# Performance work log

Measured on AMD Instinct MI355X. Metric: run time of the kernel, lower is better.

The kernel has to match this reference:

```python
import jax, jax.numpy as jnp
import numpy as np

SQRT_QKV_DIM = 8.0  # sqrt(qkv_dim=64)


def setup_inputs() -> dict:
    key = jax.random.key(0)
    ks = jax.random.split(key, 8)
    B, H, T, M, d, hid = 4, 16, 512, 512, 64, 16
    return {
        "q": jax.random.normal(ks[0], (B, H, T, d), dtype=jnp.float32),
        "k": jax.random.normal(ks[1], (B, H, M, d), dtype=jnp.float32),
        "v": jax.random.normal(ks[2], (B, H, M, d), dtype=jnp.float32),
        "D_TM": jax.random.uniform(ks[3], (B, T, M), dtype=jnp.float32),
        "mix1_weight": jax.random.uniform(ks[4], (H, 2, hid), minval=-0.7071, maxval=0.7071, dtype=jnp.float32),
        "mix1_bias": jax.random.uniform(ks[5], (H, hid), minval=-0.7071, maxval=0.7071, dtype=jnp.float32),
        "mix2_weight": jax.random.uniform(ks[6], (H, hid, 1), minval=-0.25, maxval=0.25, dtype=jnp.float32),
        "mix2_bias": jax.random.uniform(ks[7], (H, 1), minval=-0.25, maxval=0.25, dtype=jnp.float32),
    }


def reference(q, k, v, D_TM, mix1_weight, mix1_bias, mix2_weight, mix2_bias):
    B, H, T, d = q.shape
    Mc = k.shape[2]
    # scaled dot-product score: (B,H,T,M)
    dot_score = jnp.einsum("bhtd,bhmd->bhtm", q, k) / SQRT_QKV_DIM
    # per-head 2->hidden->1 MLP mixing dot score and distance bias.
    # Avoid explicit stack: linear layer over the 2 score channels expands as
    # dot*W1[:,0,:] + D*W1[:,1,:].  ms1: (B,H,T,M,hid)
    w1_dot = mix1_weight[:, 0, :][None, :, None, None, :]   # (1,H,1,1,hid)
    w1_dist = mix1_weight[:, 1, :][None, :, None, None, :]
    ms1 = (dot_score[..., None] * w1_dot
           + D_TM[:, None, :, :, None] * w1_dist
           + mix1_bias[None, :, None, None, :])
    ms1 = jax.nn.relu(ms1)
    # hidden -> 1: mixed_scores (B,H,T,M)
    mixed = jnp.einsum("bhtmc,hc->bhtm", ms1, mix2_weight[:, :, 0])
    mixed = mixed + mix2_bias[:, 0][None, :, None, None]
    weights = jax.nn.softmax(mixed, axis=3)
    out = jnp.einsum("bhtm,bhmd->bhtd", weights, v)   # (B,H,T,d)
    return out.transpose(0, 2, 1, 3).reshape(B, T, H * d)
```

## Files before the change

### kernel.cpp

```cpp
#include <hip/hip_runtime.h>
#include <stdint.h>

typedef __attribute__((ext_vector_type(8))) short short8;
typedef __attribute__((ext_vector_type(4))) float floatx4;

#define MFMA(a, b, c) __builtin_amdgcn_mfma_f32_16x16x32_bf16(a, b, c, 0, 0, 0)

union Frag { uint32_t u[4]; short8 s; };

__device__ __forceinline__ void packsplit(float a, float b, uint32_t& hi, uint32_t& lo) {
    uint32_t ua = __float_as_uint(a), ub = __float_as_uint(b);
    uint32_t ha = ua & 0xFFFF0000u, hb = ub & 0xFFFF0000u;
    float ra = a - __uint_as_float(ha);
    float rb = b - __uint_as_float(hb);
    hi = __builtin_amdgcn_perm(ub, ua, 0x07060302u);
    lo = __builtin_amdgcn_perm(__float_as_uint(rb), __float_as_uint(ra), 0x07060302u);
}

__device__ __forceinline__ float fexp2(float x) {
#if __has_builtin(__builtin_amdgcn_exp2f)
    return __builtin_amdgcn_exp2f(x);
#else
    return exp2f(x);
#endif
}

__device__ __forceinline__ void bar_lds() {
    asm volatile("s_waitcnt lgkmcnt(0)" ::: "memory");
    __builtin_amdgcn_s_barrier();
    __builtin_amdgcn_sched_barrier(0);
}


__global__ __launch_bounds__(512)
void msmha_flash(const float* __restrict__ qg, const float* __restrict__ kg,
                 const float* __restrict__ vg, const float* __restrict__ Dg,
                 const float* __restrict__ m1w, const float* __restrict__ m1b,
                 const float* __restrict__ m2w, const float* __restrict__ m2b,
                 float* __restrict__ outg) {
    __shared__ __align__(16) uint32_t sm[18432];
    __shared__ __align__(16) float4 wlds[16];

    const int tid   = threadIdx.x;
    const int w     = tid >> 6;
    const int group = w >> 2;
    const int gw    = w & 3;
    const int lane  = tid & 63;
    const int col   = lane & 15;
    const int quad  = lane >> 4;
    const int gtid  = tid & 255;

    const int bid = blockIdx.x;
    const int wgT = bid >> 6;
    const int bh  = bid & 63;
    const int h   = bh & 15;
    const int b   = bh >> 4;
    const int t0g = wgT * 64;

    const size_t base = (size_t)bh * 512 * 64;
    const float LOG2E = 1.4426950408889634f;

    if (tid < 16) {
        const float w1d = m1w[h * 32 + tid];
        const float w1s = m1w[h * 32 + 16 + tid];
        const float b1  = m1b[h * 16 + tid];
        const float w2  = m2w[h * 16 + tid];
        wlds[tid] = make_float4(w1d * (0.125f * LOG2E), w1s * LOG2E, b1 * LOG2E, 0.5f * w2);
    }

    const int ml0  = gtid >> 4;
    const int k4   = gtid & 15;
    const int dgrp = gtid & 15;
    const int m4   = gtid >> 4;
    const int cpV  = (2 * m4 + 8 * ((dgrp >> 1) & 3)) & 31;
    const int rsel = col >> 3;

    const int gb = group * 9216;
    uint32_t* KH = sm + gb;
    uint32_t* KL = sm + gb + 2304;
    uint32_t* VH = sm + gb + 4608;
    uint32_t* VL = sm + gb + 6912;

    const int moff = group * 256;
    const float* kc = kg + base + (size_t)moff * 64;
    const float* vc = vg + base + (size_t)moff * 64;
    const float* Dc = Dg + ((size_t)b * 512 + t0g + gw * 16 + col) * 512 + moff + quad * 4;

    float4 kp[4];
#pragma unroll
    for (int it = 0; it < 4; ++it)
        kp[it] = *(const float4*)(kc + (size_t)(ml0 + it * 16) * 64 + k4 * 4);

    float sA = 0.f, sB = 0.f, sC = 0.f;
#pragma unroll 1
    for (int c = 0; c < 16; ++c) {
        const float w2 = m2w[h * 16 + c];
        sA = fmaf(w2, m1w[h * 32 + c], sA);
        sB = fmaf(w2, m1w[h * 32 + 16 + c], sB);
        sC = fmaf(w2, m1b[h * 16 + c], sC);
    }
    const float Ac = sA * (0.0625f * LOG2E);
    const float Bc = sB * (0.5f * LOG2E);
    const float Cc = fmaf(0.5f, sC, m2b[h]) * LOG2E;

    Frag qh[2], ql[2];
    {
        const float* qrow = qg + base + (size_t)(t0g + gw * 16 + col) * 64;
#pragma unroll
        for (int ks = 0; ks < 2; ++ks) {
            const float4 f0 = *(const float4*)(qrow + ks * 32 + quad * 8);
            const float4 f1 = *(const float4*)(qrow + ks * 32 + quad * 8 + 4);
            packsplit(f0.x, f0.y, qh[ks].u[0], ql[ks].u[0]);
            packsplit(f0.z, f0.w, qh[ks].u[1], ql[ks].u[1]);
            packsplit(f1.x, f1.y, qh[ks].u[2], ql[ks].u[2]);
            packsplit(f1.z, f1.w, qh[ks].u[3], ql[ks].u[3]);
        }
    }

    float run_m = -3.0e38f, run_l = 0.f;
    floatx4 oacc[4];
#pragma unroll
    for (int dt = 0; dt < 4; ++dt) oacc[dt] = floatx4{0.f, 0.f, 0.f, 0.f};

#pragma unroll
    for (int mc = 0; mc < 4; ++mc) {
        float4 vp[4], dp[4];
#pragma unroll
        for (int i = 0; i < 4; ++i)
            vp[i] = *(const float4*)(vc + (size_t)(mc * 64 + 4 * m4 + i) * 64 + dgrp * 4);
#pragma unroll
        for (int mt = 0; mt < 4; ++mt)
            dp[mt] = *(const float4*)(Dc + mc * 64 + mt * 16);

#pragma unroll
        for (int it = 0; it < 4; ++it) {
            uint32_t h0, l0, h1, l1;
            packsplit(kp[it].x, kp[it].y, h0, l0);
            packsplit(kp[it].z, kp[it].w, h1, l1);
            const int ml = ml0 + it * 16;
            *(uint2*)(KH + ml * 36 + 2 * k4) = make_uint2(h0, h1);
            *(uint2*)(KL + ml * 36 + 2 * k4) = make_uint2(l0, l1);
        }
        if (mc < 3) {
            const float* kn = kc + (size_t)(mc + 1) * 64 * 64;
#pragma unroll
            for (int it = 0; it < 4; ++it)
                kp[it] = *(const float4*)(kn + (size_t)(ml0 + it * 16) * 64 + k4 * 4);
        }
        bar_lds();

        floatx4 sc[4];
        __builtin_amdgcn_s_setprio(1);
#pragma unroll
        for (int mt = 0; mt < 4; ++mt) {
            floatx4 acc = {0.f, 0.f, 0.f, 0.f};
#pragma unroll
            for (int ks = 0; ks < 2; ++ks) {
                const int ro = (mt * 16 + col) * 36 + 16 * ks + 4 * quad;
                Frag ah, al;
                ah.s = *(const short8*)(KH + ro);
                al.s = *(const short8*)(KL + ro);
                acc = MFMA(ah.s, qh[ks].s, acc);
                acc = MFMA(ah.s, ql[ks].s, acc);
                acc = MFMA(al.s, qh[ks].s, acc);
            }
            sc[mt] = acc;
        }
        __builtin_amdgcn_s_setprio(0);

#pragma unroll
        for (int jj = 0; jj < 4; ++jj) {
            uint32_t h0, l0, h1, l1;
            packsplit(((const float*)&vp[0])[jj], ((const float*)&vp[1])[jj], h0, l0);
            packsplit(((const float*)&vp[2])[jj], ((const float*)&vp[3])[jj], h1, l1);
            const int d = 4 * dgrp + jj;
            *(uint2*)(VH + d * 36 + cpV) = make_uint2(h0, h1);
            *(uint2*)(VL + d * 36 + cpV) = make_uint2(l0, l1);
        }

        float dvf[16];
#pragma unroll
        for (int mt = 0; mt < 4; ++mt) {
            dvf[mt * 4 + 0] = dp[mt].x; dvf[mt * 4 + 1] = dp[mt].y;
            dvf[mt * 4 + 2] = dp[mt].z; dvf[mt * 4 + 3] = dp[mt].w;
        }
        float mix[16];
#pragma unroll
        for (int e = 0; e < 16; ++e) mix[e] = fmaf(dvf[e], Bc, Cc);
#pragma unroll 4
        for (int c = 0; c < 16; ++c) {
            const float4 wv = wlds[c];
#pragma unroll
            for (int mt = 0; mt < 4; ++mt)
#pragma unroll
                for (int r = 0; r < 4; ++r) {
                    const float hh = fmaf(sc[mt][r], wv.x, fmaf(dvf[mt * 4 + r], wv.y, wv.z));
                    mix[mt * 4 + r] = fmaf(fabsf(hh), wv.w, mix[mt * 4 + r]);
                }
        }
#pragma unroll
        for (int mt = 0; mt < 4; ++mt)
#pragma unroll
            for (int r = 0; r < 4; ++r)
                sc[mt][r] = fmaf(sc[mt][r], Ac, mix[mt * 4 + r]);

        float cmx = -3.0e38f;
#pragma unroll
        for (int mt = 0; mt < 4; ++mt)
#pragma unroll
            for (int r = 0; r < 4; ++r) cmx = fmaxf(cmx, sc[mt][r]);
        cmx = fmaxf(cmx, __shfl_xor(cmx, 16, 64));
        cmx = fmaxf(cmx, __shfl_xor(cmx, 32, 64));
        const float nm    = fmaxf(run_m, cmx);
        const float scale = fexp2(run_m - nm);
        float csum = 0.f;
#pragma unroll
        for (int mt = 0; mt < 4; ++mt)
#pragma unroll
            for (int r = 0; r < 4; ++r) {
                const float p = fexp2(sc[mt][r] - nm);
                sc[mt][r] = p;
                csum += p;
            }
        csum += __shfl_xor(csum, 16, 64);
        csum += __shfl_xor(csum, 32, 64);
        run_l = fmaf(run_l, scale, csum);
        run_m = nm;
        float sOT[4];
#pragma unroll
        for (int r = 0; r < 4; ++r) sOT[r] = __shfl(scale, quad * 4 + r, 64);
#pragma unroll
        for (int dt = 0; dt < 4; ++dt)
#pragma unroll
            for (int r = 0; r < 4; ++r) oacc[dt][r] *= sOT[r];

        bar_lds();

        const int prow = (gw * 16 + col) * 36;
#pragma unroll
        for (int mt = 0; mt < 4; ++mt) {
            uint32_t h0, l0, h1, l1;
            packsplit(sc[mt][0], sc[mt][1], h0, l0);
            packsplit(sc[mt][2], sc[mt][3], h1, l1);
            *(uint2*)(KH + prow + mt * 8 + 2 * quad) = make_uint2(h0, h1);
            *(uint2*)(KL + prow + mt * 8 + 2 * quad) = make_uint2(l0, l1);
        }

        __builtin_amdgcn_s_setprio(1);
#pragma unroll
        for (int ks = 0; ks < 2; ++ks) {
            const int po = prow + 16 * ks + 4 * quad;
            Frag pah, pal;
            pah.s = *(const short8*)(KH + po);
            pal.s = *(const short8*)(KL + po);
#pragma unroll
            for (int dt = 0; dt < 4; ++dt) {
                const int cbd = ((16 * ks + 4 * quad) + 8 * ((2 * dt + rsel) & 3)) & 31;
                const int vo = (dt * 16 + col) * 36 + cbd;
                Frag bhv, blv;
                bhv.s = *(const short8*)(VH + vo);
                blv.s = *(const short8*)(VL + vo);
                oacc[dt] = MFMA(pah.s, bhv.s, oacc[dt]);
                oacc[dt] = MFMA(pah.s, blv.s, oacc[dt]);
                oacc[dt] = MFMA(pal.s, bhv.s, oacc[dt]);
            }
        }
        __builtin_amdgcn_s_setprio(0);

        bar_lds();
    }

    float* smf = (float*)sm;
    if (group == 1) {
        if (quad == 0) {
            smf[13376 + gw * 16 + col] = run_m;
            smf[13440 + gw * 16 + col] = run_l;
        }
        const int t = gw * 16 + quad * 4;
#pragma unroll
        for (int dt = 0; dt < 4; ++dt)
#pragma unroll
            for (int r = 0; r < 4; ++r)
                smf[9216 + (t + r) * 65 + dt * 16 + col] = oacc[dt][r];
    }
    bar_lds();
    if (group == 0) {
        const float m1c = smf[13376 + gw * 16 + col];
        const float l1c = smf[13440 + gw * 16 + col];
        const float M   = fmaxf(run_m, m1c);
        const float s0  = fexp2(run_m - M);
        const float s1  = fexp2(m1c - M);
        const float rdn = 1.f / fmaf(run_l, s0, l1c * s1);
        float s0T[4], s1T[4], rdT[4];
#pragma unroll
        for (int r = 0; r < 4; ++r) {
            s0T[r] = __shfl(s0, quad * 4 + r, 64);
            s1T[r] = __shfl(s1, quad * 4 + r, 64);
            rdT[r] = __shfl(rdn, quad * 4 + r, 64);
        }
        const int t = gw * 16 + quad * 4;
        const size_t obase = ((size_t)b * 512 + t0g + t) * 1024 + h * 64 + col;
#pragma unroll
        for (int dt = 0; dt < 4; ++dt)
#pragma unroll
            for (int r = 0; r < 4; ++r) {
                const float o1 = smf[9216 + (t + r) * 65 + dt * 16 + col];
                outg[obase + (size_t)r * 1024 + dt * 16] =
                    fmaf(oacc[dt][r], s0T[r], o1 * s1T[r]) * rdT[r];
            }
    }
}

extern "C" void kernel_launch(void* const* d_in, const int* in_sizes, int n_in,
                              void* d_out, int out_size, void* d_ws, size_t ws_size,
                              hipStream_t stream) {
    const float* q   = (const float*)d_in[0];
    const float* k   = (const float*)d_in[1];
    const float* v   = (const float*)d_in[2];
    const float* dtm = (const float*)d_in[3];
    const float* m1w = (const float*)d_in[4];
    const float* m1b = (const float*)d_in[5];
    const float* m2w = (const float*)d_in[6];
    const float* m2b = (const float*)d_in[7];
    float* out = (float*)d_out;

    dim3 grid(4 * 16 * 8);
    dim3 block(512);
    msmha_flash<<<grid, block, 0, stream>>>(q, k, v, dtm, m1w, m1b, m2w, m2b, out);
}
```

Before: 136.9 us.

## Swizzle K/P LDS tiles, pack MLP math into float2, drop loop-end barrier

The K and P tiles in LDS switch from a padded stride-36 layout to an XOR-swizzled stride-32 layout, which shrinks shared memory while still aiming to avoid bank conflicts. K loading is reassigned so each wave writes exactly the K rows it later overwrites with its own P rows. That makes the per-iteration trailing barrier unnecessary, so it moves out of the loop. The per-element score MLP, max and scaling are rewritten on float2 vectors so the compiler can emit packed FMA/max instructions. The risk is subtle correctness in the barrier removal and swizzle indexing, plus register-pressure changes from the vectorized form.

```diff
diff --git a/kernel.cpp b/kernel.cpp
--- a/kernel.cpp
+++ b/kernel.cpp
@@ -3,6 +3,7 @@
 
 typedef __attribute__((ext_vector_type(8))) short short8;
 typedef __attribute__((ext_vector_type(4))) float floatx4;
+typedef __attribute__((ext_vector_type(2))) float float2v;
 
 #define MFMA(a, b, c) __builtin_amdgcn_mfma_f32_16x16x32_bf16(a, b, c, 0, 0, 0)
 
@@ -38,7 +39,7 @@
                  const float* __restrict__ m1w, const float* __restrict__ m1b,
                  const float* __restrict__ m2w, const float* __restrict__ m2b,
                  float* __restrict__ outg) {
-    __shared__ __align__(16) uint32_t sm[18432];
+    __shared__ __align__(16) uint32_t sm[17408];
     __shared__ __align__(16) float4 wlds[16];
 
     const int tid   = threadIdx.x;
@@ -68,18 +69,20 @@
         wlds[tid] = make_float4(w1d * (0.125f * LOG2E), w1s * LOG2E, b1 * LOG2E, 0.5f * w2);
     }
 
-    const int ml0  = gtid >> 4;
-    const int k4   = gtid & 15;
+    const int krow = 16 * gw + (lane >> 2);
+    const int kqt  = lane & 3;
+    const int ksw  = (krow & 7) << 2;
+    const int rsw  = (col & 7) << 2;
     const int dgrp = gtid & 15;
     const int m4   = gtid >> 4;
     const int cpV  = (2 * m4 + 8 * ((dgrp >> 1) & 3)) & 31;
     const int rsel = col >> 3;
 
-    const int gb = group * 9216;
+    const int gb = group * 8704;
     uint32_t* KH = sm + gb;
-    uint32_t* KL = sm + gb + 2304;
-    uint32_t* VH = sm + gb + 4608;
-    uint32_t* VL = sm + gb + 6912;
+    uint32_t* KL = sm + gb + 2048;
+    uint32_t* VH = sm + gb + 4096;
+    uint32_t* VL = sm + gb + 6400;
 
     const int moff = group * 256;
     const float* kc = kg + base + (size_t)moff * 64;
@@ -88,8 +91,8 @@
 
     float4 kp[4];
 #pragma unroll
-    for (int it = 0; it < 4; ++it)
-        kp[it] = *(const float4*)(kc + (size_t)(ml0 + it * 16) * 64 + k4 * 4);
+    for (int i = 0; i < 4; ++i)
+        kp[i] = *(const float4*)(kc + (size_t)krow * 64 + 16 * i + 4 * kqt);
 
     float sA = 0.f, sB = 0.f, sC = 0.f;
 #pragma unroll 1
@@ -122,6 +125,8 @@
 #pragma unroll
     for (int dt = 0; dt < 4; ++dt) oacc[dt] = floatx4{0.f, 0.f, 0.f, 0.f};
 
+    const float2v Ac2 = {Ac, Ac}, Bc2 = {Bc, Bc}, Cc2 = {Cc, Cc};
+
 #pragma unroll
     for (int mc = 0; mc < 4; ++mc) {
         float4 vp[4], dp[4];
@@ -133,19 +138,18 @@
             dp[mt] = *(const float4*)(Dc + mc * 64 + mt * 16);
 
 #pragma unroll
-        for (int it = 0; it < 4; ++it) {
+        for (int i = 0; i < 4; ++i) {
             uint32_t h0, l0, h1, l1;
-            packsplit(kp[it].x, kp[it].y, h0, l0);
-            packsplit(kp[it].z, kp[it].w, h1, l1);
-            const int ml = ml0 + it * 16;
-            *(uint2*)(KH + ml * 36 + 2 * k4) = make_uint2(h0, h1);
-            *(uint2*)(KL + ml * 36 + 2 * k4) = make_uint2(l0, l1);
+            packsplit(kp[i].x, kp[i].y, h0, l0);
+            packsplit(kp[i].z, kp[i].w, h1, l1);
+            const int off = (8 * i + 2 * kqt) ^ ksw;
+            *(uint2*)(KH + krow * 32 + off) = make_uint2(h0, h1);
+            *(uint2*)(KL + krow * 32 + off) = make_uint2(l0, l1);
         }
         if (mc < 3) {
-            const float* kn = kc + (size_t)(mc + 1) * 64 * 64;
-#pragma unroll
-            for (int it = 0; it < 4; ++it)
-                kp[it] = *(const float4*)(kn + (size_t)(ml0 + it * 16) * 64 + k4 * 4);
+#pragma unroll
+            for (int i = 0; i < 4; ++i)
+                kp[i] = *(const float4*)(kc + (size_t)((mc + 1) * 64 + krow) * 64 + 16 * i + 4 * kqt);
         }
         bar_lds();
 
@@ -156,7 +160,7 @@
             floatx4 acc = {0.f, 0.f, 0.f, 0.f};
 #pragma unroll
             for (int ks = 0; ks < 2; ++ks) {
-                const int ro = (mt * 16 + col) * 36 + 16 * ks + 4 * quad;
+                const int ro = (mt * 16 + col) * 32 + ((16 * ks + 4 * quad) ^ rsw);
                 Frag ah, al;
                 ah.s = *(const short8*)(KH + ro);
                 al.s = *(const short8*)(KL + ro);
@@ -178,50 +182,48 @@
             *(uint2*)(VL + d * 36 + cpV) = make_uint2(l0, l1);
         }
 
-        float dvf[16];
+        float2v scp[8], dvp[8], mixp[8];
 #pragma unroll
         for (int mt = 0; mt < 4; ++mt) {
-            dvf[mt * 4 + 0] = dp[mt].x; dvf[mt * 4 + 1] = dp[mt].y;
-            dvf[mt * 4 + 2] = dp[mt].z; dvf[mt * 4 + 3] = dp[mt].w;
-        }
-        float mix[16];
-#pragma unroll
-        for (int e = 0; e < 16; ++e) mix[e] = fmaf(dvf[e], Bc, Cc);
+            scp[2 * mt]     = float2v{sc[mt][0], sc[mt][1]};
+            scp[2 * mt + 1] = float2v{sc[mt][2], sc[mt][3]};
+            dvp[2 * mt]     = float2v{dp[mt].x, dp[mt].y};
+            dvp[2 * mt + 1] = float2v{dp[mt].z, dp[mt].w};
+        }
+#pragma unroll
+        for (int e = 0; e < 8; ++e) mixp[e] = dvp[e] * Bc2 + Cc2;
 #pragma unroll 4
         for (int c = 0; c < 16; ++c) {
             const float4 wv = wlds[c];
-#pragma unroll
-            for (int mt = 0; mt < 4; ++mt)
-#pragma unroll
-                for (int r = 0; r < 4; ++r) {
-                    const float hh = fmaf(sc[mt][r], wv.x, fmaf(dvf[mt * 4 + r], wv.y, wv.z));
-                    mix[mt * 4 + r] = fmaf(fabsf(hh), wv.w, mix[mt * 4 + r]);
-                }
-        }
-#pragma unroll
-        for (int mt = 0; mt < 4; ++mt)
-#pragma unroll
-            for (int r = 0; r < 4; ++r)
-                sc[mt][r] = fmaf(sc[mt][r], Ac, mix[mt * 4 + r]);
-
-        float cmx = -3.0e38f;
-#pragma unroll
-        for (int mt = 0; mt < 4; ++mt)
-#pragma unroll
-            for (int r = 0; r < 4; ++r) cmx = fmaxf(cmx, sc[mt][r]);
+            const float2v wx = {wv.x, wv.x}, wy = {wv.y, wv.y};
+            const float2v wz = {wv.z, wv.z}, ww = {wv.w, wv.w};
+#pragma unroll
+            for (int e = 0; e < 8; ++e) {
+                const float2v hh = scp[e] * wx + (dvp[e] * wy + wz);
+                const float2v ah = __builtin_elementwise_max(hh, -hh);
+                mixp[e] = ah * ww + mixp[e];
+            }
+        }
+#pragma unroll
+        for (int e = 0; e < 8; ++e) scp[e] = scp[e] * Ac2 + mixp[e];
+
+        float2v m2 = scp[0];
+#pragma unroll
+        for (int e = 1; e < 8; ++e) m2 = __builtin_elementwise_max(m2, scp[e]);
+        float cmx = fmaxf(m2.x, m2.y);
         cmx = fmaxf(cmx, __shfl_xor(cmx, 16, 64));
         cmx = fmaxf(cmx, __shfl_xor(cmx, 32, 64));
         const float nm    = fmaxf(run_m, cmx);
         const float scale = fexp2(run_m - nm);
-        float csum = 0.f;
-#pragma unroll
-        for (int mt = 0; mt < 4; ++mt)
-#pragma unroll
-            for (int r = 0; r < 4; ++r) {
-                const float p = fexp2(sc[mt][r] - nm);
-                sc[mt][r] = p;
-                csum += p;
-            }
+        float csx = 0.f, csy = 0.f;
+#pragma unroll
+        for (int e = 0; e < 8; ++e) {
+            const float px = fexp2(scp[e].x - nm);
+            const float py = fexp2(scp[e].y - nm);
+            scp[e] = float2v{px, py};
+            csx += px; csy += py;
+        }
+        float csum = csx + csy;
         csum += __shfl_xor(csum, 16, 64);
         csum += __shfl_xor(csum, 32, 64);
         run_l = fmaf(run_l, scale, csum);
@@ -229,27 +231,27 @@
         float sOT[4];
 #pragma unroll
         for (int r = 0; r < 4; ++r) sOT[r] = __shfl(scale, quad * 4 + r, 64);
-#pragma unroll
-        for (int dt = 0; dt < 4; ++dt)
-#pragma unroll
-            for (int r = 0; r < 4; ++r) oacc[dt][r] *= sOT[r];
+        const floatx4 sv = {sOT[0], sOT[1], sOT[2], sOT[3]};
+#pragma unroll
+        for (int dt = 0; dt < 4; ++dt) oacc[dt] *= sv;
 
         bar_lds();
 
-        const int prow = (gw * 16 + col) * 36;
+        const int prow = (gw * 16 + col) * 32;
 #pragma unroll
         for (int mt = 0; mt < 4; ++mt) {
             uint32_t h0, l0, h1, l1;
-            packsplit(sc[mt][0], sc[mt][1], h0, l0);
-            packsplit(sc[mt][2], sc[mt][3], h1, l1);
-            *(uint2*)(KH + prow + mt * 8 + 2 * quad) = make_uint2(h0, h1);
-            *(uint2*)(KL + prow + mt * 8 + 2 * quad) = make_uint2(l0, l1);
+            packsplit(scp[2 * mt].x, scp[2 * mt].y, h0, l0);
+            packsplit(scp[2 * mt + 1].x, scp[2 * mt + 1].y, h1, l1);
+            const int off = (mt * 8 + 2 * quad) ^ rsw;
+            *(uint2*)(KH + prow + off) = make_uint2(h0, h1);
+            *(uint2*)(KL + prow + off) = make_uint2(l0, l1);
         }
 
         __builtin_amdgcn_s_setprio(1);
 #pragma unroll
         for (int ks = 0; ks < 2; ++ks) {
-            const int po = prow + 16 * ks + 4 * quad;
+            const int po = prow + ((16 * ks + 4 * quad) ^ rsw);
             Frag pah, pal;
             pah.s = *(const short8*)(KH + po);
             pal.s = *(const short8*)(KL + po);
@@ -266,27 +268,27 @@
             }
         }
         __builtin_amdgcn_s_setprio(0);
-
-        bar_lds();
-    }
+    }
+
+    bar_lds();
 
     float* smf = (float*)sm;
     if (group == 1) {
         if (quad == 0) {
-            smf[13376 + gw * 16 + col] = run_m;
-            smf[13440 + gw * 16 + col] = run_l;
+            smf[12864 + gw * 16 + col] = run_m;
+            smf[12928 + gw * 16 + col] = run_l;
         }
         const int t = gw * 16 + quad * 4;
 #pragma unroll
         for (int dt = 0; dt < 4; ++dt)
 #pragma unroll
             for (int r = 0; r < 4; ++r)
-                smf[9216 + (t + r) * 65 + dt * 16 + col] = oacc[dt][r];
+                smf[8704 + (t + r) * 65 + dt * 16 + col] = oacc[dt][r];
     }
     bar_lds();
     if (group == 0) {
-        const float m1c = smf[13376 + gw * 16 + col];
-        const float l1c = smf[13440 + gw * 16 + col];
+        const float m1c = smf[12864 + gw * 16 + col];
+        const float l1c = smf[12928 + gw * 16 + col];
         const float M   = fmaxf(run_m, m1c);
         const float s0  = fexp2(run_m - M);
         const float s1  = fexp2(m1c - M);
@@ -304,7 +306,7 @@
         for (int dt = 0; dt < 4; ++dt)
 #pragma unroll
             for (int r = 0; r < 4; ++r) {
-                const float o1 = smf[9216 + (t + r) * 65 + dt * 16 + col];
+                const float o1 = smf[8704 + (t + r) * 65 + dt * 16 + col];
                 outg[obase + (size_t)r * 1024 + dt * 16] =
                     fmaf(oacc[dt][r], s0T[r], o1 * s1T[r]) * rdT[r];
             }
```

Result: faster. 132.4 us (-3.3%).
